# Kernel optimization log

Hardware: AMD Instinct MI355X
Metric: run time of the kernel (lower is better)

Reference implementation:

```python
import jax, jax.numpy as jnp
import numpy as np

SHIFT = 1  # original picks +/-1 randomly at init; fixed to +1 for determinism

def setup_inputs() -> dict:
    key = jax.random.key(0)
    k1, k2, k3 = jax.random.split(key, 3)
    return {
        "x": jax.random.normal(k1, (1, 128, 56, 56), dtype=jnp.float32),
        "w1": jax.random.normal(k2, (4, 64, 3), dtype=jnp.float32),   # weights[0]
        "w2": jax.random.normal(k3, (32, 2, 3), dtype=jnp.float32),   # weights[1]
    }

def reference(x, w1, w2):
    # roll along H within the (64, 2) channel split
    t = x.reshape(1, 64, 2, 56, 56)
    t = jnp.roll(t, SHIFT, axis=3)
    t = t.reshape(1, 128, 56, 56)
    # unfold kernel (3,1), padding (1,0): 3-tap windows over H
    tp = jnp.pad(t, ((0, 0), (0, 0), (1, 1), (0, 0)))
    t3 = jnp.stack([tp[:, :, j:j + 56, :] for j in range(3)], axis=2)  # (1,128,3,56,56) = (C, kernel, H, W)
    t3 = t3.reshape(1, 64, 2, 3, 56, 56)  # (l, i=64, o=2, j=3, m, n) matches torch unfold C-then-kernel order
    t4 = jnp.einsum('liojmn,kij->lkomn', t3, w1)  # (1, 4, 2, 56, 56)
    # second unfold: torch reshapes t4 to (1,448,56,1) so the 3-tap window slides over n (last axis)
    tp2 = jnp.pad(t4, ((0, 0), (0, 0), (0, 0), (0, 0), (1, 1)))
    t5 = jnp.stack([tp2[..., j:j + 56] for j in range(3)], axis=4)  # (1,4,2,56,3,56) = (l,o,j,m,k,n)
    t6 = jnp.einsum('lojmkn,ijk->liomn', t5, w2)  # (1, 32, 4, 56, 56)
    return t6.reshape(1, 128, 56, 56)
```

## Files before the change

kernel.cpp:

```cpp
#include <hip/hip_runtime.h>


#define HH 56
#define WW 56

__global__ __launch_bounds__(256) void fused_shift_conv(
    const float* __restrict__ x,
    const float* __restrict__ w1,
    const float* __restrict__ w2,
    float* __restrict__ out)
{
    __shared__ float w1s[64 * 12];
    __shared__ float w2s[192];
    __shared__ float t4s[2][4][WW + 2];

    const int tid = threadIdx.x;
    const int m = blockIdx.x;

    for (int idx = tid; idx < 768; idx += 256) {
        int k = idx / 192;
        int r = idx - k * 192;
        int i = r / 3;
        int j = r - i * 3;
        w1s[i * 12 + j * 4 + k] = w1[idx];
    }
    if (tid < 192) w2s[tid] = w2[tid];
    if (tid < 16) {
        int o = tid >> 3;
        int k = (tid >> 1) & 3;
        int side = tid & 1;
        t4s[o][k][side * (WW + 1)] = 0.0f;
    }
    __syncthreads();

    if (tid < 112) {
        const int n = tid % 56;
        const int o = tid / 56;
        float acc0 = 0.f, acc1 = 0.f, acc2 = 0.f, acc3 = 0.f;
        #pragma unroll
        for (int j = 0; j < 3; ++j) {
            const int h_t = m + j - 1;
            if (h_t >= 0 && h_t < HH) {
                int h_src = h_t - 1;
                if (h_src < 0) h_src += HH;
                const float* xp = x + (size_t)h_src * WW + n + (size_t)o * (HH * WW);
                #pragma unroll 8
                for (int i = 0; i < 64; ++i) {
                    const float xv = xp[(size_t)i * 2 * (HH * WW)];
                    const float* wp = &w1s[i * 12 + j * 4];
                    acc0 += xv * wp[0];
                    acc1 += xv * wp[1];
                    acc2 += xv * wp[2];
                    acc3 += xv * wp[3];
                }
            }
        }
        t4s[o][0][n + 1] = acc0;
        t4s[o][1][n + 1] = acc1;
        t4s[o][2][n + 1] = acc2;
        t4s[o][3][n + 1] = acc3;
    }
    __syncthreads();

    for (int item = tid; item < 128 * WW; item += 256) {
        const int cc = item / WW;
        const int n = item - cc * WW;
        const int i32 = cc >> 2;
        const int k4 = cc & 3;
        const float* wp = &w2s[i32 * 6];
        const float s = t4s[0][k4][n]     * wp[0]
                      + t4s[0][k4][n + 1] * wp[1]
                      + t4s[0][k4][n + 2] * wp[2]
                      + t4s[1][k4][n]     * wp[3]
                      + t4s[1][k4][n + 1] * wp[4]
                      + t4s[1][k4][n + 2] * wp[5];
        out[(size_t)cc * (HH * WW) + (size_t)m * WW + n] = s;
    }
}

extern "C" void kernel_launch(void* const* d_in, const int* in_sizes, int n_in,
                              void* d_out, int out_size, void* d_ws, size_t ws_size,
                              hipStream_t stream) {
    const float* x  = (const float*)d_in[0];
    const float* w1 = (const float*)d_in[1];
    const float* w2 = (const float*)d_in[2];
    float* out = (float*)d_out;
    fused_shift_conv<<<dim3(HH), dim3(256), 0, stream>>>(x, w1, w2, out);
}
```

Baseline: 71.50 us.

## Split rows into column tiles and parallelize channel reduction across threads

```diff
diff --git a/kernel.cpp b/kernel.cpp
--- a/kernel.cpp
+++ b/kernel.cpp
@@ -3,8 +3,9 @@
 
 #define HH 56
 #define WW 56
+#define HW (HH * WW)
 
-__global__ __launch_bounds__(256) void fused_shift_conv(
+__global__ __launch_bounds__(512) void fused_shift_conv2(
     const float* __restrict__ x,
     const float* __restrict__ w1,
     const float* __restrict__ w2,
@@ -12,12 +13,14 @@
 {
     __shared__ float w1s[64 * 12];
     __shared__ float w2s[192];
-    __shared__ float t4s[2][4][WW + 2];
+    __shared__ float part[16][2][16][4];
+    __shared__ float t4s[2][4][16];
 
     const int tid = threadIdx.x;
-    const int m = blockIdx.x;
+    const int m  = blockIdx.y;
+    const int n0 = blockIdx.x * 14;
 
-    for (int idx = tid; idx < 768; idx += 256) {
+    for (int idx = tid; idx < 768; idx += 512) {
         int k = idx / 192;
         int r = idx - k * 192;
         int i = r / 3;
@@ -25,56 +28,63 @@
         w1s[i * 12 + j * 4 + k] = w1[idx];
     }
     if (tid < 192) w2s[tid] = w2[tid];
-    if (tid < 16) {
-        int o = tid >> 3;
-        int k = (tid >> 1) & 3;
-        int side = tid & 1;
-        t4s[o][k][side * (WW + 1)] = 0.0f;
-    }
     __syncthreads();
 
-    if (tid < 112) {
-        const int n = tid % 56;
-        const int o = tid / 56;
-        float acc0 = 0.f, acc1 = 0.f, acc2 = 0.f, acc3 = 0.f;
+    const int nl = tid & 15;
+    const int o  = (tid >> 4) & 1;
+    const int ic = tid >> 5;
+    const int n_g = n0 + nl - 1;
+
+    float a0 = 0.f, a1 = 0.f, a2 = 0.f, a3 = 0.f;
+    if (n_g >= 0 && n_g < WW) {
         #pragma unroll
         for (int j = 0; j < 3; ++j) {
             const int h_t = m + j - 1;
             if (h_t >= 0 && h_t < HH) {
                 int h_src = h_t - 1;
                 if (h_src < 0) h_src += HH;
-                const float* xp = x + (size_t)h_src * WW + n + (size_t)o * (HH * WW);
-                #pragma unroll 8
-                for (int i = 0; i < 64; ++i) {
-                    const float xv = xp[(size_t)i * 2 * (HH * WW)];
-                    const float* wp = &w1s[i * 12 + j * 4];
-                    acc0 += xv * wp[0];
-                    acc1 += xv * wp[1];
-                    acc2 += xv * wp[2];
-                    acc3 += xv * wp[3];
+                const float* xp = x + (size_t)(ic * 8 + o) * HW
+                                    + (size_t)h_src * WW + n_g;
+                #pragma unroll
+                for (int ii = 0; ii < 4; ++ii) {
+                    const float xv = xp[(size_t)ii * 2 * HW];
+                    const float* wp = &w1s[(ic * 4 + ii) * 12 + j * 4];
+                    a0 += xv * wp[0];
+                    a1 += xv * wp[1];
+                    a2 += xv * wp[2];
+                    a3 += xv * wp[3];
                 }
             }
         }
-        t4s[o][0][n + 1] = acc0;
-        t4s[o][1][n + 1] = acc1;
-        t4s[o][2][n + 1] = acc2;
-        t4s[o][3][n + 1] = acc3;
+    }
+    ((float4*)part)[tid] = make_float4(a0, a1, a2, a3);
+    __syncthreads();
+
+    if (tid < 128) {
+        const int k  = tid & 3;
+        const int n  = (tid >> 2) & 15;
+        const int oo = tid >> 6;
+        float s = 0.f;
+        #pragma unroll
+        for (int c = 0; c < 16; ++c)
+            s += part[c][oo][n][k];
+        t4s[oo][k][n] = s;
     }
     __syncthreads();
 
-    for (int item = tid; item < 128 * WW; item += 256) {
-        const int cc = item / WW;
-        const int n = item - cc * WW;
+    for (int item = tid; item < 128 * 14; item += 512) {
+        const int cc = item / 14;
+        const int nn = item - cc * 14;
         const int i32 = cc >> 2;
         const int k4 = cc & 3;
         const float* wp = &w2s[i32 * 6];
-        const float s = t4s[0][k4][n]     * wp[0]
-                      + t4s[0][k4][n + 1] * wp[1]
-                      + t4s[0][k4][n + 2] * wp[2]
-                      + t4s[1][k4][n]     * wp[3]
-                      + t4s[1][k4][n + 1] * wp[4]
-                      + t4s[1][k4][n + 2] * wp[5];
-        out[(size_t)cc * (HH * WW) + (size_t)m * WW + n] = s;
+        const float s = t4s[0][k4][nn]     * wp[0]
+                      + t4s[0][k4][nn + 1] * wp[1]
+                      + t4s[0][k4][nn + 2] * wp[2]
+                      + t4s[1][k4][nn]     * wp[3]
+                      + t4s[1][k4][nn + 1] * wp[4]
+                      + t4s[1][k4][nn + 2] * wp[5];
+        out[(size_t)cc * HW + (size_t)m * WW + (n0 + nn)] = s;
     }
 }
 
@@ -85,5 +95,5 @@
     const float* w1 = (const float*)d_in[1];
     const float* w2 = (const float*)d_in[2];
     float* out = (float*)d_out;
-    fused_shift_conv<<<dim3(HH), dim3(256), 0, stream>>>(x, w1, w2, out);
+    fused_shift_conv2<<<dim3(4, 56), dim3(512), 0, stream>>>(x, w1, w2, out);
 }
```

Result: faster. 60.27 us (-15.7%).
